# Performance work log

Hardware: AMD Instinct MI355X
Metric: run time of the kernel (lower is better)

The kernel has to match this reference:

```python
import jax, jax.numpy as jnp
import numpy as np

B, T, H = 256, 48, 512   # batch, timesteps, hidden (= size_seq feature dim)
S = H                    # size_seq == hidden feature dim (dim_seq_in = S+1)
K = 4                    # k_wk_ahead


def setup_inputs() -> dict:
    key = jax.random.key(0)
    ks = jax.random.split(key, 20)
    g = lambda k, shp: (jax.random.normal(k, shp, dtype=jnp.float32) * 0.05)
    inp = {
        "hiddens": jax.random.normal(ks[0], (B, T, S), dtype=jnp.float32),
        "allys": jax.random.normal(ks[1], (B, T), dtype=jnp.float32),
        "k_wk_ahead": K,
        # InputAttention params (Linear stored as [in, out])
        "Wh": g(ks[2], (H, S)), "bh": g(ks[3], (S,)),
        "Ws": g(ks[4], (S, S)), "bs": g(ks[5], (S,)),
        "Wo": g(ks[6], (S, 1)), "bo": g(ks[7], (1,)),
        # GRU params (torch layout: [3H, in]/[3H, H], gates ordered r,z,n)
        "W_ih": g(ks[8], (3 * H, S + 1)), "W_hh": g(ks[9], (3 * H, H)),
        "b_ih": g(ks[10], (3 * H,)), "b_hh": g(ks[11], (3 * H,)),
        # out_layer MLP: H->H/2->H/4->H/8->1 with LeakyReLU after each
        "W1": g(ks[12], (H, H // 2)), "b1": g(ks[13], (H // 2,)),
        "W2": g(ks[14], (H // 2, H // 4)), "b2": g(ks[15], (H // 4,)),
        "W3": g(ks[16], (H // 4, H // 8)), "b3": g(ks[17], (H // 8,)),
        "W4": g(ks[18], (H // 8, 1)), "b4": g(ks[19], (1,)),
    }
    return inp


def _gru_step(x, h, W_ih, W_hh, b_ih, b_hh):
    # torch GRU cell: gates ordered (reset, update, new)
    gi = x @ W_ih.T + b_ih          # [B, 3H]
    gh = h @ W_hh.T + b_hh          # [B, 3H]
    ir, iz, inn = jnp.split(gi, 3, axis=-1)
    hr, hz, hn = jnp.split(gh, 3, axis=-1)
    r = jax.nn.sigmoid(ir + hr)
    z = jax.nn.sigmoid(iz + hz)
    n = jnp.tanh(inn + r * hn)
    return (1.0 - z) * n + z * h


def reference(hiddens, allys, k_wk_ahead, Wh, bh, Ws, bs, Wo, bo,
              W_ih, W_hh, b_ih, b_hh, W1, b1, W2, b2, W3, b3, W4, b4):
    Bb, Tt, Ss = hiddens.shape
    # linearSignals(hiddens) is time-step-invariant: precompute once
    ls = hiddens @ Ws + bs                      # [B, T, S]

    def step(d_prev, ally_t):
        lh = d_prev @ Wh + bh                   # [B, S]
        e = jnp.tanh(lh[:, None, :] + ls) @ Wo + bo    # [B, T, 1]
        att = jax.nn.softmax(e, axis=1)[..., 0]        # [B, T]
        c = jnp.einsum('bt,bts->bs', att, hiddens)     # [B, S]
        x = jnp.concatenate([c, ally_t[:, None]], axis=1)   # [B, S+1]
        d = _gru_step(x, d_prev, W_ih, W_hh, b_ih, b_hh)
        return d, c

    d0 = jnp.zeros((Bb, W_hh.shape[1]), dtype=hiddens.dtype)
    d_last, cs = jax.lax.scan(step, d0, jnp.swapaxes(allys, 0, 1))
    c_last = cs[-1]                             # c_vectors[:, -1]

    def mlp(d):
        h = jax.nn.leaky_relu(d @ W1 + b1)
        h = jax.nn.leaky_relu(h @ W2 + b2)
        h = jax.nn.leaky_relu(h @ W3 + b3)
        return jax.nn.leaky_relu(h @ W4 + b4)   # dropout is identity in eval

    outs = []
    last_d = d_last
    for _ in range(k_wk_ahead):
        out = mlp(last_d)                       # [B, 1]
        outs.append(out)
        x = jnp.concatenate([c_last, out], axis=1)
        last_d = _gru_step(x, last_d, W_ih, W_hh, b_ih, b_hh)
    return jnp.stack(outs, axis=1)[..., 0]      # [B, K]
```

## Files before the change

kernel.cpp:

```cpp
#include <hip/hip_runtime.h>
#include <cstdio>

#ifndef __has_builtin
#define __has_builtin(x) 0
#endif

#define NB      256
#define NT      48
#define NS      512
#define KAHEAD  4
#define NTHREADS 1024
#define NBLOCKS  256
#define GSIZE    32
#define RSTRIDE  544
#define XSLOT    512
#define XROWB    1088

#define WS_D     0
#define WS_X     139264
#define WS_LH    278528
#define WS_BAR   409600
#define WS_WA    409856
#define WS_WC    934144
#define WS_WN    1196288
#define WS_WS    1327360
#define WS_WAL   1458432
#define WS_FLOATS 1982720

#define L_XHI    0
#define L_XLO    34816
#define L_LSB    69632
#define L_GH     118784
#define L_GI     125312
#define L_LH     131840
#define L_WO     133888
#define L_E      135936
#define L_ATT    136192
#define L_CP     136448
#define L_H1P    138496
#define L_H1S    142592
#define L_H2P    143616
#define L_H2S    145664
#define L_H3P    146176
#define L_MISC   147200
#define L_PB     147216
#define LDS_BYTES 155408

typedef float    f4v  __attribute__((ext_vector_type(4)));
typedef float    f16v __attribute__((ext_vector_type(16)));
typedef _Float16 h4v  __attribute__((ext_vector_type(4)));
typedef _Float16 h8v  __attribute__((ext_vector_type(8)));

__device__ __forceinline__ f16v MFMA32(h8v a, h8v b, f16v c) {
    return __builtin_amdgcn_mfma_f32_32x32x16_f16(a, b, c, 0, 0, 0);
}
__device__ __forceinline__ f4v MFMA16(h8v a, h8v b, f4v c) {
    return __builtin_amdgcn_mfma_f32_16x16x32_f16(a, b, c, 0, 0, 0);
}

#if __has_builtin(__builtin_bit_cast)
#define F2H_BITS(v) __builtin_bit_cast(h8v, (v))
#define H2F_BITS(v) __builtin_bit_cast(f4v, (v))
#else
__device__ __forceinline__ h8v f2h_bits_(f4v v) { union { f4v f; h8v h; } u; u.f = v; return u.h; }
__device__ __forceinline__ f4v h2f_bits_(h8v v) { union { f4v f; h8v h; } u; u.h = v; return u.f; }
#define F2H_BITS(v) f2h_bits_(v)
#define H2F_BITS(v) h2f_bits_(v)
#endif

__device__ __forceinline__ float frcp_(float x) {
#if __has_builtin(__builtin_amdgcn_rcpf)
    return __builtin_amdgcn_rcpf(x);
#else
    return 1.0f / x;
#endif
}
__device__ __forceinline__ float ftanh_(float x) {
    float e = __expf(2.0f * x);
    return 1.0f - 2.0f * frcp_(e + 1.0f);
}
__device__ __forceinline__ float fsig_(float x) { return frcp_(1.0f + __expf(-x)); }
__device__ __forceinline__ float lrelu_(float x) { return fmaxf(x, 0.01f * x); }
__device__ __forceinline__ void split16_(float v, _Float16& hi, _Float16& lo) {
    _Float16 h = (_Float16)v;
    hi = h;
    lo = (_Float16)(v - (float)h);
}
__device__ __forceinline__ unsigned short f2hbits_(float v) {
    union { _Float16 h; unsigned short u; } c; c.h = (_Float16)v; return c.u;
}
__device__ __forceinline__ float hbits2f_(unsigned short u) {
    union { unsigned short u; _Float16 h; } c; c.u = u; return (float)c.h;
}

__device__ __forceinline__ void cstore1(float* p, float v) {
    asm volatile("global_store_dword %0, %1, off sc0" :: "v"(p), "v"(v) : "memory");
}
__device__ __forceinline__ f4v cload4(const float* p) {
    f4v v;
    asm volatile("global_load_dwordx4 %0, %1, off sc0" : "=v"(v) : "v"(p));
    return v;
}
__device__ __forceinline__ float cload1(const float* p) {
    float v;
    asm volatile("global_load_dword %0, %1, off sc0" : "=v"(v) : "v"(p));
    return v;
}
__device__ __forceinline__ void cwait() {
    asm volatile("s_waitcnt vmcnt(0)" ::: "memory");
    __builtin_amdgcn_sched_barrier(0);
}

__device__ __forceinline__ void gbar(unsigned* bar, unsigned* epoch) {
    asm volatile("s_waitcnt vmcnt(0)" ::: "memory");
    __syncthreads();
    if (threadIdx.x == 0) {
        *epoch += GSIZE;
        __hip_atomic_fetch_add(bar, 1u, __ATOMIC_RELAXED, __HIP_MEMORY_SCOPE_AGENT);
        unsigned target = *epoch;
        int guard = 0;
        while (__hip_atomic_load(bar, __ATOMIC_RELAXED, __HIP_MEMORY_SCOPE_AGENT) < target) {
#if __has_builtin(__builtin_amdgcn_s_sleep)
            __builtin_amdgcn_s_sleep(1);
#endif
            if (++guard > (1 << 17)) break;
        }
    }
    __syncthreads();
}

__device__ __forceinline__ void cvtStore_(char* hiB, char* loB, int idx, f4v v) {
    unsigned row = (unsigned)idx / 544u;
    unsigned col = (unsigned)idx - row * 544u;
    h4v h, l;
    #pragma unroll
    for (int i = 0; i < 4; ++i) { _Float16 hh, ll; split16_(v[i], hh, ll); h[i] = hh; l[i] = ll; }
    *(h4v*)(hiB + row * XROWB + col * 2) = h;
    *(h4v*)(loB + row * XROWB + col * 2) = l;
}
__device__ __forceinline__ void stagePanel(const float* __restrict__ gsrc,
                                           char* __restrict__ hiB,
                                           char* __restrict__ loB, int tid) {
    f4v v0 = cload4(gsrc + tid * 4);
    f4v v1 = cload4(gsrc + 4096 + tid * 4);
    f4v v2 = cload4(gsrc + 8192 + tid * 4);
    f4v v3 = cload4(gsrc + 12288 + tid * 4);
    f4v v4 = {0.f, 0.f, 0.f, 0.f};
    if (tid < 256) v4 = cload4(gsrc + 16384 + tid * 4);
    cwait();
    cvtStore_(hiB, loB, tid * 4, v0);
    cvtStore_(hiB, loB, 4096 + tid * 4, v1);
    cvtStore_(hiB, loB, 8192 + tid * 4, v2);
    cvtStore_(hiB, loB, 12288 + tid * 4, v3);
    if (tid < 256) cvtStore_(hiB, loB, 16384 + tid * 4, v4);
}

#define DO_GEMMA(doLH) do {                                                          \
    f16v acc_ = (f16v){0,0,0,0,0,0,0,0,0,0,0,0,0,0,0,0};                             \
    if (w < 4) {                                                                     \
        const int kc_ = w >> 1;                                                      \
        const int aoff_ = (l & 31) * XROWB + ((l >> 5) << 4);                        \
        _Pragma("unroll")                                                            \
        for (int kt = 0; kt < 16; ++kt) {                                            \
            h8v ah = *(const h8v*)(smem + L_XHI + aoff_ + (kc_ * 16 + kt) * 32);     \
            h8v al = *(const h8v*)(smem + L_XLO + aoff_ + (kc_ * 16 + kt) * 32);     \
            acc_ = MFMA32(ah, wreg[kt], acc_);                                       \
            acc_ = MFMA32(al, wreg[kt], acc_);                                       \
        }                                                                            \
        const _Float16* blp_ = walF +                                                \
            ((long)((cix * 2 + (w & 1)) * 32 + kc_ * 16)) * 512 + (l << 3);          \
        _Pragma("unroll 4")                                                          \
        for (int kt = 0; kt < 16; ++kt) {                                            \
            h8v ah = *(const h8v*)(smem + L_XHI + aoff_ + (kc_ * 16 + kt) * 32);     \
            h8v bl8 = *(const h8v*)(blp_ + kt * 512);                                \
            acc_ = MFMA32(ah, bl8, acc_);                                            \
        }                                                                            \
        if (kc_ == 1) {                                                              \
            _Pragma("unroll")                                                        \
            for (int r = 0; r < 16; ++r) pbuf[(w & 1) * 1024 + r * 64 + l] = acc_[r];\
        }                                                                            \
    }                                                                                \
    __syncthreads();                                                                 \
    if (w < 2) {                                                                     \
        _Pragma("unroll")                                                            \
        for (int r = 0; r < 16; ++r) acc_[r] += pbuf[w * 1024 + r * 64 + l];         \
        const int c_ = w * 32 + (l & 31);                                            \
        const int rb_ = (l >> 5) << 2;                                               \
        if (c_ < 16) {                                                               \
            if (doLH) {                                                              \
                const int j_ = cix * 16 + c_;                                        \
                const float bb_ = bh[j_];                                            \
                _Pragma("unroll")                                                    \
                for (int r = 0; r < 16; ++r) {                                       \
                    int row_ = (r & 3) + ((r >> 2) << 3) + rb_;                      \
                    cstore1(lhw + (long)(g * 32 + row_) * NS + j_, acc_[r] + bb_);   \
                }                                                                    \
            }                                                                        \
        } else {                                                                     \
            const int gate_ = (c_ - 16) >> 4, jj_ = (c_ - 16) & 15;                  \
            const float bb_ = b_hh[gate_ * 512 + cix * 16 + jj_];                    \
            _Pragma("unroll")                                                        \
            for (int r = 0; r < 16; ++r) {                                           \
                int row_ = (r & 3) + ((r >> 2) << 3) + rb_;                          \
                ghs[gate_ * 544 + row_ * 17 + jj_] = acc_[r] + bb_;                  \
            }                                                                        \
        }                                                                            \
    }                                                                                \
} while (0)

#define DO_GEMMC() do {                                                              \
    f16v acc_ = (f16v){0,0,0,0,0,0,0,0,0,0,0,0,0,0,0,0};                             \
    f4v an0_ = {0.f,0.f,0.f,0.f}, an1_ = {0.f,0.f,0.f,0.f};                          \
    if (w == 4 || w == 5) {                                                          \
        const int kc_ = w - 4;                                                       \
        const int aoff_ = (l & 31) * XROWB + ((l >> 5) << 4);                        \
        _Pragma("unroll")                                                            \
        for (int kt = 0; kt < 16; ++kt) {                                            \
            h8v ah = *(const h8v*)(smem + L_XHI + aoff_ + (kc_ * 16 + kt) * 32);     \
            h8v al = *(const h8v*)(smem + L_XLO + aoff_ + (kc_ * 16 + kt) * 32);     \
            acc_ = MFMA32(ah, wreg[kt], acc_);                                       \
            acc_ = MFMA32(al, wreg[kt], acc_);                                       \
        }                                                                            \
        if (kc_ == 1) {                                                              \
            _Pragma("unroll")                                                        \
            for (int r = 0; r < 16; ++r) pbuf[r * 64 + l] = acc_[r];                 \
        }                                                                            \
    } else if (w == 6 || w == 7) {                                                   \
        const int kc_ = w - 6;                                                       \
        const int a0_ = (l & 15) * XROWB + ((l >> 4) << 4);                          \
        const int a1_ = a0_ + 16 * XROWB;                                            \
        _Pragma("unroll")                                                            \
        for (int kt = 0; kt < 8; ++kt) {                                             \
            const int kb_ = (kc_ * 8 + kt) * 64;                                     \
            h8v ah0 = *(const h8v*)(smem + L_XHI + a0_ + kb_);                       \
            h8v al0 = *(const h8v*)(smem + L_XLO + a0_ + kb_);                       \
            h8v ah1 = *(const h8v*)(smem + L_XHI + a1_ + kb_);                       \
            h8v al1 = *(const h8v*)(smem + L_XLO + a1_ + kb_);                       \
            an0_ = MFMA16(ah0, wreg[kt], an0_); an0_ = MFMA16(al0, wreg[kt], an0_);  \
            an1_ = MFMA16(ah1, wreg[kt], an1_); an1_ = MFMA16(al1, wreg[kt], an1_);  \
        }                                                                            \
        if (kc_ == 1) {                                                              \
            _Pragma("unroll")                                                        \
            for (int r = 0; r < 4; ++r) {                                            \
                pbuf[1024 + r * 64 + l] = an0_[r];                                   \
                pbuf[1280 + r * 64 + l] = an1_[r];                                   \
            }                                                                        \
        }                                                                            \
    }                                                                                \
    __syncthreads();                                                                 \
    if (w == 4) {                                                                    \
        _Pragma("unroll")                                                            \
        for (int r = 0; r < 16; ++r) acc_[r] += pbuf[r * 64 + l];                    \
        const int c_ = l & 31, gate_ = c_ >> 4, jj_ = c_ & 15;                       \
        const int rb_ = (l >> 5) << 2;                                               \
        const float bb_ = b_ih[gate_ * 512 + cix * 16 + jj_];                        \
        _Pragma("unroll")                                                            \
        for (int r = 0; r < 16; ++r) {                                               \
            int row_ = (r & 3) + ((r >> 2) << 3) + rb_;                              \
            gis[gate_ * 544 + row_ * 17 + jj_] = acc_[r] + bb_;                      \
        }                                                                            \
    } else if (w == 6) {                                                             \
        const int jj_ = l & 15;                                                      \
        const float bb_ = b_ih[1024 + cix * 16 + jj_];                               \
        _Pragma("unroll")                                                            \
        for (int r = 0; r < 4; ++r) {                                                \
            int row_ = ((l >> 4) << 2) + r;                                          \
            gis[1088 + row_ * 17 + jj_] = an0_[r] + pbuf[1024 + r * 64 + l] + bb_;   \
            gis[1088 + (16 + row_) * 17 + jj_] = an1_[r] + pbuf[1280 + r * 64 + l] + bb_; \
        }                                                                            \
    }                                                                                \
} while (0)

__device__ __forceinline__ void lsGemm(const char* smem, const _Float16* WS_,
        int tid, int ch, unsigned short* lsb, const float* bs) {
    const int w = tid >> 6, l = tid & 63;
    const int mt = w & 1, ng = w >> 1;
    const int aoff = (mt * 16 + (l & 15)) * XROWB + ((l >> 4) << 4);
    f4v acc[4] = {{0,0,0,0},{0,0,0,0},{0,0,0,0},{0,0,0,0}};
    for (int kt = 0; kt < 16; ++kt) {
        h8v ah = *(const h8v*)(smem + L_XHI + aoff + kt * 64);
        h8v al = *(const h8v*)(smem + L_XLO + aoff + kt * 64);
        #pragma unroll
        for (int i = 0; i < 4; ++i) {
            const _Float16* bp = WS_ + ((long)((ng * 4 + i) * 16 + kt)) * 512 + (l << 3);
            h8v bb = *(const h8v*)bp;
            acc[i] = MFMA16(ah, bb, acc[i]);
            acc[i] = MFMA16(al, bb, acc[i]);
        }
    }
    #pragma unroll
    for (int i = 0; i < 4; ++i) {
        const int n = (ng * 4 + i) * 16 + (l & 15);
        const float bsv = bs[n];
        #pragma unroll
        for (int r = 0; r < 4; ++r) {
            int row = mt * 16 + ((l >> 4) << 2) + r;
            if (row < 24)
                lsb[(ch * 24 + row) * NS + n] = f2hbits_(acc[i][r] + bsv);
        }
    }
}

__global__ void prep_kernel(const float* __restrict__ Whh,
                            const float* __restrict__ Wih,
                            const float* __restrict__ Wh,
                            const float* __restrict__ Ws,
                            float* __restrict__ ws) {
    long i = (long)blockIdx.x * blockDim.x + threadIdx.x;
    long stride = (long)gridDim.x * blockDim.x;
    _Float16* wa  = (_Float16*)(ws + WS_WA);
    _Float16* wal = (_Float16*)(ws + WS_WAL);
    _Float16* wc  = (_Float16*)(ws + WS_WC);
    _Float16* wn  = (_Float16*)(ws + WS_WN);
    _Float16* wsls = (_Float16*)(ws + WS_WS);

    for (long p = i; p < 131072; p += stride) {
        int l = (int)(p & 63);
        long t = p >> 6;
        int kt = (int)(t & 31);
        int u = (int)(t >> 5);
        int nt = u & 1, cix = u >> 1;
        int c = nt * 32 + (l & 31);
        #pragma unroll
        for (int e = 0; e < 8; ++e) {
            int k = kt * 16 + ((l >> 5) << 3) + e;
            float wv;
            if (c < 16) wv = Wh[(long)k * 512 + cix * 16 + c];
            else {
                int gate = (c - 16) >> 4, j = cix * 16 + ((c - 16) & 15);
                wv = Whh[((long)(gate * 512 + j)) * 512 + k];
            }
            _Float16 hv = (_Float16)wv;
            wa[p * 8 + e]  = hv;
            wal[p * 8 + e] = (_Float16)(wv - (float)hv);
        }
    }
    for (long p = i; p < 65536; p += stride) {
        int l = (int)(p & 63);
        long t = p >> 6;
        int kt = (int)(t & 31), cix = (int)(t >> 5);
        int c = l & 31, gate = c >> 4, j = cix * 16 + (c & 15);
        #pragma unroll
        for (int e = 0; e < 8; ++e) {
            int k = kt * 16 + ((l >> 5) << 3) + e;
            wc[p * 8 + e] = (_Float16)Wih[((long)(gate * 512 + j)) * 513 + k];
        }
    }
    for (long p = i; p < 32768; p += stride) {
        int l = (int)(p & 63);
        long t = p >> 6;
        int kt = (int)(t & 15), cix = (int)(t >> 4);
        int j = cix * 16 + (l & 15);
        #pragma unroll
        for (int e = 0; e < 8; ++e) {
            int k = kt * 32 + ((l >> 4) << 3) + e;
            wn[p * 8 + e] = (_Float16)Wih[((long)(1024 + j)) * 513 + k];
        }
    }
    for (long p = i; p < 32768; p += stride) {
        int l = (int)(p & 63);
        long t = p >> 6;
        int kt = (int)(t & 15), nt = (int)(t >> 4);
        int n = nt * 16 + (l & 15);
        #pragma unroll
        for (int e = 0; e < 8; ++e) {
            int k = kt * 32 + ((l >> 4) << 3) + e;
            wsls[p * 8 + e] = (_Float16)Ws[(long)k * 512 + n];
        }
    }
    for (long p = i; p < 278528; p += stride) ws[WS_D + p] = 0.0f;
    if (i < 256) ((unsigned*)(ws + WS_BAR))[i] = 0u;
}

__global__ void __launch_bounds__(NTHREADS, 4) fused_kernel(
        const float* __restrict__ hiddens, const float* __restrict__ allys,
        const float* __restrict__ bs,
        const float* __restrict__ Wo, const float* __restrict__ bo,
        const float* __restrict__ bh,
        const float* __restrict__ b_ih, const float* __restrict__ b_hh,
        const float* __restrict__ Wih,
        const float* __restrict__ W1, const float* __restrict__ b1,
        const float* __restrict__ W2, const float* __restrict__ b2,
        const float* __restrict__ W3, const float* __restrict__ b3,
        const float* __restrict__ W4, const float* __restrict__ b4,
        float* __restrict__ ws, float* __restrict__ out) {
    const int tid = threadIdx.x;

    float* dw  = ws + WS_D;
    float* xw  = ws + WS_X;
    float* lhw = ws + WS_LH;
    const _Float16* waF  = (const _Float16*)(ws + WS_WA);
    const _Float16* walF = (const _Float16*)(ws + WS_WAL);
    const _Float16* wcF  = (const _Float16*)(ws + WS_WC);
    const _Float16* wnF  = (const _Float16*)(ws + WS_WN);
    const _Float16* wsF  = (const _Float16*)(ws + WS_WS);
    unsigned* barbase = (unsigned*)(ws + WS_BAR);

    extern __shared__ char smem[];
    char*           xhi   = smem + L_XHI;
    char*           xlo   = smem + L_XLO;
    unsigned short* lsb   = (unsigned short*)(smem + L_LSB);
    float*          ghs   = (float*)(smem + L_GH);
    float*          gis   = (float*)(smem + L_GI);
    float*          lh_s  = (float*)(smem + L_LH);
    float*          wo_s  = (float*)(smem + L_WO);
    float*          e_s   = (float*)(smem + L_E);
    float*          att_s = (float*)(smem + L_ATT);
    float*          h1p   = (float*)(smem + L_H1P);
    float*          h1s   = (float*)(smem + L_H1S);
    float*          h2p   = (float*)(smem + L_H2P);
    float*          h2s   = (float*)(smem + L_H2S);
    float*          h3p   = (float*)(smem + L_H3P);
    int*            misc  = (int*)(smem + L_MISC);
    float*          pbuf  = (float*)(smem + L_PB);

    if (tid == 0) {
        unsigned xcc;
        asm volatile("s_getreg_b32 %0, hwreg(HW_REG_XCC_ID)" : "=s"(xcc));
        int gx = (int)(xcc & 7u);
        unsigned rk = __hip_atomic_fetch_add(barbase + gx * 32 + 1, 1u,
                                             __ATOMIC_RELAXED, __HIP_MEMORY_SCOPE_AGENT);
        misc[0] = gx;
        misc[1] = (int)(rk & 31u);
    }
    __syncthreads();
    const int g = misc[0], cix = misc[1];
    const int myb = g * 32 + cix;
    unsigned* bar = barbase + (g << 5);
    unsigned epoch = 0;

    const int w = tid >> 6, l = tid & 63;
    const int sS = tid & 511;
    const int rowE = tid >> 4, jE = tid & 15;
    const int jgE = cix * 16 + jE;
    const float* gPanelD = dw + (long)g * GSIZE * RSTRIDE;
    const float* gPanelX = xw + (long)g * GSIZE * RSTRIDE;

    float w512r = 0.f, w512z = 0.f, w512n = 0.f;
    if (tid < 512) {
        w512r = Wih[(long)jgE * 513 + 512];
        w512z = Wih[(long)(512 + jgE) * 513 + 512];
        w512n = Wih[(long)(1024 + jgE) * 513 + 512];
    }

    if (tid < NS) wo_s[tid] = Wo[tid];

    for (int i = tid; i < 4352; i += NTHREADS) *(f4v*)(smem + i * 16) = (f4v){0,0,0,0};
    for (int ch = 0; ch < 2; ++ch) {
        __syncthreads();
        {
            const float* src = hiddens + ((long)myb * NT + ch * 24) * NS;
            const int i0 = tid * 12;
            #pragma unroll
            for (int j3 = 0; j3 < 3; ++j3) {
                int idx = i0 + j3 * 4;
                f4v v = *(const f4v*)(src + idx);
                int row = idx >> 9, col = idx & 511;
                h4v h, lo;
                #pragma unroll
                for (int e = 0; e < 4; ++e) { _Float16 hh, ll; split16_(v[e], hh, ll); h[e] = hh; lo[e] = ll; }
                *(h4v*)(xhi + row * XROWB + col * 2) = h;
                *(h4v*)(xlo + row * XROWB + col * 2) = lo;
            }
        }
        __syncthreads();
        lsGemm(smem, wsF, tid, ch, lsb, bs);
    }
    __syncthreads();

    h8v wreg[16];
    if (w < 4) {
        const _Float16* p = waF + ((long)((cix * 2 + (w & 1)) * 32 + (w >> 1) * 16)) * 512 + (l << 3);
        #pragma unroll
        for (int kt = 0; kt < 16; ++kt) wreg[kt] = *(const h8v*)(p + kt * 512);
    } else if (w < 6) {
        const _Float16* p = wcF + ((long)(cix * 32 + (w - 4) * 16)) * 512 + (l << 3);
        #pragma unroll
        for (int kt = 0; kt < 16; ++kt) wreg[kt] = *(const h8v*)(p + kt * 512);
    } else if (w < 8) {
        const _Float16* p = wnF + ((long)(cix * 16 + (w - 6) * 8)) * 512 + (l << 3);
        #pragma unroll
        for (int kt = 0; kt < 8; ++kt) wreg[kt] = *(const h8v*)(p + kt * 512);
    } else {
        const float* hb = hiddens + (long)myb * NT * NS + sS;
        #pragma unroll
        for (int q = 0; q < 12; ++q) {
            f4v v = { hb[(q * 4 + 0) * 512], hb[(q * 4 + 1) * 512],
                      hb[(q * 4 + 2) * 512], hb[(q * 4 + 3) * 512] };
            wreg[q] = F2H_BITS(v);
        }
    }

    const float bo0 = bo[0];

    for (int t = 0; t < NT; ++t) {
        stagePanel(gPanelD, xhi, xlo, tid);
        __syncthreads();
        DO_GEMMA(true);
        gbar(bar, &epoch);

        if (tid < 128) {
            f4v v = cload4(lhw + (long)myb * NS + tid * 4);
            cwait();
            *(f4v*)(lh_s + tid * 4) = v;
        }
        if (tid == 0) cstore1(xw + (long)myb * RSTRIDE + XSLOT, allys[myb * NT + t]);
        __syncthreads();
        {
            const int wv = tid >> 6, ln = tid & 63;
            for (int q = 0; q < 3; ++q) {
                const int tt = wv * 3 + q;
                float p = 0.f;
                #pragma unroll
                for (int i2 = 0; i2 < 8; ++i2) {
                    int s = ln + (i2 << 6);
                    p = fmaf(wo_s[s], ftanh_(lh_s[s] + hbits2f_(lsb[tt * NS + s])), p);
                }
                #pragma unroll
                for (int off = 32; off >= 1; off >>= 1) p += __shfl_xor(p, off, 64);
                if (ln == 0) e_s[tt] = p + bo0;
            }
        }
        __syncthreads();
        if (tid < 64) {
            float v = (tid < NT) ? e_s[tid] : -1e30f;
            float m = v;
            #pragma unroll
            for (int off = 32; off >= 1; off >>= 1) m = fmaxf(m, __shfl_xor(m, off, 64));
            float ex = (tid < NT) ? __expf(v - m) : 0.0f;
            float ssum = ex;
            #pragma unroll
            for (int off = 32; off >= 1; off >>= 1) ssum += __shfl_xor(ssum, off, 64);
            if (tid < NT) att_s[tid] = ex * frcp_(ssum);
        }
        __syncthreads();
        if (tid >= 512) {
            float c = 0.f;
            #pragma unroll
            for (int q = 0; q < 12; ++q) {
                f4v hv = H2F_BITS(wreg[q]);
                c = fmaf(att_s[q * 4 + 0], hv.x, c);
                c = fmaf(att_s[q * 4 + 1], hv.y, c);
                c = fmaf(att_s[q * 4 + 2], hv.z, c);
                c = fmaf(att_s[q * 4 + 3], hv.w, c);
            }
            cstore1(xw + (long)myb * RSTRIDE + sS, c);
        }
        gbar(bar, &epoch);

        float hp = 0.f;
        if (tid < 512) hp = cload1(dw + (long)(g * 32 + rowE) * RSTRIDE + jgE);
        stagePanel(gPanelX, xhi, xlo, tid);
        __syncthreads();
        DO_GEMMC();
        __syncthreads();
        if (tid < 512) {
            float x512f = (float)*(const _Float16*)(xhi + rowE * XROWB + 1024)
                        + (float)*(const _Float16*)(xlo + rowE * XROWB + 1024);
            float gr  = fmaf(x512f, w512r, gis[rowE * 17 + jE]        + ghs[rowE * 17 + jE]);
            float gz  = fmaf(x512f, w512z, gis[544 + rowE * 17 + jE]  + ghs[544 + rowE * 17 + jE]);
            float gni = fmaf(x512f, w512n, gis[1088 + rowE * 17 + jE]);
            float gnh = ghs[1088 + rowE * 17 + jE];
            float rg = fsig_(gr);
            float zg = fsig_(gz);
            float ng = ftanh_(fmaf(rg, gnh, gni));
            cstore1(dw + (long)(g * 32 + rowE) * RSTRIDE + jgE, (1.f - zg) * ng + zg * hp);
        }
        gbar(bar, &epoch);
    }

    for (int kk = 0; kk < KAHEAD; ++kk) {
        {
            float v = 0.f;
            if (tid < NS) v = cload1(dw + (long)myb * RSTRIDE + tid);
            cwait();
            if (tid < NS) lh_s[tid] = v;
        }
        __syncthreads();
        {
            int n = tid & 255, q4 = tid >> 8;
            const float* av = lh_s + q4 * 128;
            const float* wp = W1 + (long)(q4 * 128) * 256 + n;
            float acc = 0.f;
            #pragma unroll 4
            for (int k2 = 0; k2 < 128; ++k2) { acc = fmaf(av[k2], wp[0], acc); wp += 256; }
            h1p[n * 4 + q4] = acc;
        }
        __syncthreads();
        if (tid < 256) {
            float v = h1p[tid * 4] + h1p[tid * 4 + 1] + h1p[tid * 4 + 2] + h1p[tid * 4 + 3];
            h1s[tid] = lrelu_(v + b1[tid]);
        }
        __syncthreads();
        if (tid < 512) {
            int n = tid & 127, q4 = tid >> 7;
            const float* av = h1s + q4 * 64;
            const float* wp = W2 + (long)(q4 * 64) * 128 + n;
            float acc = 0.f;
            #pragma unroll 4
            for (int k2 = 0; k2 < 64; ++k2) { acc = fmaf(av[k2], wp[0], acc); wp += 128; }
            h2p[n * 4 + q4] = acc;
        }
        __syncthreads();
        if (tid < 128) {
            float v = h2p[tid * 4] + h2p[tid * 4 + 1] + h2p[tid * 4 + 2] + h2p[tid * 4 + 3];
            h2s[tid] = lrelu_(v + b2[tid]);
        }
        __syncthreads();
        if (tid < 256) {
            int n = tid & 63, q4 = tid >> 6;
            const float* av = h2s + q4 * 32;
            const float* wp = W3 + (long)(q4 * 32) * 64 + n;
            float acc = 0.f;
            #pragma unroll 4
            for (int k2 = 0; k2 < 32; ++k2) { acc = fmaf(av[k2], wp[0], acc); wp += 64; }
            h3p[n * 4 + q4] = acc;
        }
        __syncthreads();
        if (tid < 64) {
            float v = h3p[tid * 4] + h3p[tid * 4 + 1] + h3p[tid * 4 + 2] + h3p[tid * 4 + 3];
            float h3v = lrelu_(v + b3[tid]);
            float p = h3v * W4[tid];
            #pragma unroll
            for (int off = 32; off >= 1; off >>= 1) p += __shfl_xor(p, off, 64);
            if (tid == 0) {
                float o = lrelu_(p + b4[0]);
                out[myb * KAHEAD + kk] = o;
                cstore1(xw + (long)myb * RSTRIDE + XSLOT, o);
            }
        }
        if (kk < KAHEAD - 1) {
            gbar(bar, &epoch);
            float hp = 0.f;
            if (tid < 512) hp = cload1(dw + (long)(g * 32 + rowE) * RSTRIDE + jgE);
            stagePanel(gPanelD, xhi, xlo, tid);
            __syncthreads();
            DO_GEMMA(false);
            __syncthreads();
            stagePanel(gPanelX, xhi, xlo, tid);
            __syncthreads();
            DO_GEMMC();
            __syncthreads();
            if (tid < 512) {
                float x512f = (float)*(const _Float16*)(xhi + rowE * XROWB + 1024)
                            + (float)*(const _Float16*)(xlo + rowE * XROWB + 1024);
                float gr  = fmaf(x512f, w512r, gis[rowE * 17 + jE]        + ghs[rowE * 17 + jE]);
                float gz  = fmaf(x512f, w512z, gis[544 + rowE * 17 + jE]  + ghs[544 + rowE * 17 + jE]);
                float gni = fmaf(x512f, w512n, gis[1088 + rowE * 17 + jE]);
                float gnh = ghs[1088 + rowE * 17 + jE];
                float rg = fsig_(gr);
                float zg = fsig_(gz);
                float ng = ftanh_(fmaf(rg, gnh, gni));
                cstore1(dw + (long)(g * 32 + rowE) * RSTRIDE + jgE, (1.f - zg) * ng + zg * hp);
            }
            gbar(bar, &epoch);
        }
    }
}

extern "C" void kernel_launch(void* const* d_in, const int* in_sizes, int n_in,
                              void* d_out, int out_size, void* d_ws, size_t ws_size,
                              hipStream_t stream) {
    const float* hiddens = (const float*)d_in[0];
    const float* allys   = (const float*)d_in[1];
    const float* Wh   = (const float*)d_in[3];
    const float* bh   = (const float*)d_in[4];
    const float* Ws   = (const float*)d_in[5];
    const float* bs   = (const float*)d_in[6];
    const float* Wo   = (const float*)d_in[7];
    const float* bo   = (const float*)d_in[8];
    const float* W_ih = (const float*)d_in[9];
    const float* W_hh = (const float*)d_in[10];
    const float* b_ih = (const float*)d_in[11];
    const float* b_hh = (const float*)d_in[12];
    const float* W1 = (const float*)d_in[13];
    const float* b1 = (const float*)d_in[14];
    const float* W2 = (const float*)d_in[15];
    const float* b2 = (const float*)d_in[16];
    const float* W3 = (const float*)d_in[17];
    const float* b3 = (const float*)d_in[18];
    const float* W4 = (const float*)d_in[19];
    const float* b4 = (const float*)d_in[20];
    float* wsf = (float*)d_ws;
    float* outf = (float*)d_out;

    if (ws_size < (size_t)WS_FLOATS * sizeof(float)) {
        fprintf(stderr, "kernel_launch: workspace too small (%zu < %zu)\n",
                ws_size, (size_t)WS_FLOATS * sizeof(float));
        return;
    }

    prep_kernel<<<dim3(2048), dim3(256), 0, stream>>>(W_hh, W_ih, Wh, Ws, wsf);

    (void)hipFuncSetAttribute((const void*)fused_kernel,
                              hipFuncAttributeMaxDynamicSharedMemorySize, LDS_BYTES);

    void* args[] = { &hiddens, &allys, &bs, &Wo, &bo, &bh,
                     &b_ih, &b_hh, &W_ih, &W1, &b1, &W2, &b2, &W3, &b3, &W4, &b4,
                     &wsf, &outf };
    hipError_t e = hipLaunchCooperativeKernel((void*)fused_kernel,
                                              dim3(NBLOCKS), dim3(NTHREADS),
                                              args, LDS_BYTES, stream);
    if (e != hipSuccess) {
        fprintf(stderr, "coop launch failed (%d); plain fallback\n", (int)e);
        (void)hipGetLastError();
        fused_kernel<<<dim3(NBLOCKS), dim3(NTHREADS), LDS_BYTES, stream>>>(
            hiddens, allys, bs, Wo, bo, bh, b_ih, b_hh, W_ih,
            W1, b1, W2, b2, W3, b3, W4, b4, wsf, outf);
    }
}
```

Before: 1.980 ms.

## Compute attention projection locally per block, removing grid barrier and lh exchange

Each block now computes its own batch row's d_prev @ Wh with packed fp16 dot2 instructions over a new pair-packed Wh layout, on waves that were idle during the GRU hidden GEMM. This removes the global store of lh, one grid-wide barrier per timestep and the reload of lh from global memory. The low-half correction term for W_hh is dropped, so the hidden GEMM now uses single fp16 weights, trading some precision for fewer MFMAs. The LDS row stride is padded, which should reduce bank conflicts on the row reads of the new loop.

New measurement: 3.615 ms. 1.83x slower.

```diff
diff --git a/kernel.cpp b/kernel.cpp
--- a/kernel.cpp
+++ b/kernel.cpp
@@ -14,7 +14,7 @@
 #define GSIZE    32
 #define RSTRIDE  544
 #define XSLOT    512
-#define XROWB    1088
+#define XROWB    1104
 
 #define WS_D     0
 #define WS_X     139264
@@ -24,30 +24,31 @@
 #define WS_WC    934144
 #define WS_WN    1196288
 #define WS_WS    1327360
-#define WS_WAL   1458432
-#define WS_FLOATS 1982720
+#define WS_WHF   1458432
+#define WS_FLOATS 1589504
 
 #define L_XHI    0
-#define L_XLO    34816
-#define L_LSB    69632
-#define L_GH     118784
-#define L_GI     125312
-#define L_LH     131840
-#define L_WO     133888
-#define L_E      135936
-#define L_ATT    136192
-#define L_CP     136448
-#define L_H1P    138496
-#define L_H1S    142592
-#define L_H2P    143616
-#define L_H2S    145664
-#define L_H3P    146176
-#define L_MISC   147200
-#define L_PB     147216
-#define LDS_BYTES 155408
+#define L_XLO    35328
+#define L_LSB    70656
+#define L_GH     119808
+#define L_GI     126336
+#define L_LH     132864
+#define L_WO     134912
+#define L_E      136960
+#define L_ATT    137216
+#define L_CP     137472
+#define L_H1P    139520
+#define L_H1S    143616
+#define L_H2P    144640
+#define L_H2S    146688
+#define L_H3P    147200
+#define L_MISC   148224
+#define L_PB     148240
+#define LDS_BYTES 156432
 
 typedef float    f4v  __attribute__((ext_vector_type(4)));
 typedef float    f16v __attribute__((ext_vector_type(16)));
+typedef _Float16 h2v  __attribute__((ext_vector_type(2)));
 typedef _Float16 h4v  __attribute__((ext_vector_type(4)));
 typedef _Float16 h8v  __attribute__((ext_vector_type(8)));
 
@@ -67,6 +68,15 @@
 #define F2H_BITS(v) f2h_bits_(v)
 #define H2F_BITS(v) h2f_bits_(v)
 #endif
+
+__device__ __forceinline__ h2v u2h2_(unsigned u) { union { unsigned u; h2v h; } c; c.u = u; return c.h; }
+__device__ __forceinline__ float fdot2_(h2v a, h2v b, float c) {
+#if __has_builtin(__builtin_amdgcn_fdot2)
+    return __builtin_amdgcn_fdot2(a, b, c, false);
+#else
+    return fmaf((float)a[0], (float)b[0], fmaf((float)a[1], (float)b[1], c));
+#endif
+}
 
 __device__ __forceinline__ float frcp_(float x) {
 #if __has_builtin(__builtin_amdgcn_rcpf)
@@ -155,7 +165,7 @@
     if (tid < 256) cvtStore_(hiB, loB, 16384 + tid * 4, v4);
 }
 
-#define DO_GEMMA(doLH) do {                                                          \
+#define DO_GEMMA() do {                                                              \
     f16v acc_ = (f16v){0,0,0,0,0,0,0,0,0,0,0,0,0,0,0,0};                             \
     if (w < 4) {                                                                     \
         const int kc_ = w >> 1;                                                      \
@@ -167,18 +177,21 @@
             acc_ = MFMA32(ah, wreg[kt], acc_);                                       \
             acc_ = MFMA32(al, wreg[kt], acc_);                                       \
         }                                                                            \
-        const _Float16* blp_ = walF +                                                \
-            ((long)((cix * 2 + (w & 1)) * 32 + kc_ * 16)) * 512 + (l << 3);          \
-        _Pragma("unroll 4")                                                          \
-        for (int kt = 0; kt < 16; ++kt) {                                            \
-            h8v ah = *(const h8v*)(smem + L_XHI + aoff_ + (kc_ * 16 + kt) * 32);     \
-            h8v bl8 = *(const h8v*)(blp_ + kt * 512);                                \
-            acc_ = MFMA32(ah, bl8, acc_);                                            \
-        }                                                                            \
         if (kc_ == 1) {                                                              \
             _Pragma("unroll")                                                        \
             for (int r = 0; r < 16; ++r) pbuf[(w & 1) * 1024 + r * 64 + l] = acc_[r];\
         }                                                                            \
+    } else if (w < 12) {                                                             \
+        const int j_ = tid - 256;                                                    \
+        const unsigned* dru_ = (const unsigned*)(smem + L_XHI + cix * XROWB);        \
+        const unsigned* wp_ = whf2 + j_;                                             \
+        float accl_ = bh[j_];                                                        \
+        _Pragma("unroll 8")                                                          \
+        for (int k2 = 0; k2 < 256; ++k2) {                                           \
+            accl_ = fdot2_(u2h2_(dru_[k2]), u2h2_(wp_[0]), accl_);                   \
+            wp_ += 512;                                                              \
+        }                                                                            \
+        lh_s[j_] = accl_;                                                            \
     }                                                                                \
     __syncthreads();                                                                 \
     if (w < 2) {                                                                     \
@@ -186,17 +199,42 @@
         for (int r = 0; r < 16; ++r) acc_[r] += pbuf[w * 1024 + r * 64 + l];         \
         const int c_ = w * 32 + (l & 31);                                            \
         const int rb_ = (l >> 5) << 2;                                               \
-        if (c_ < 16) {                                                               \
-            if (doLH) {                                                              \
-                const int j_ = cix * 16 + c_;                                        \
-                const float bb_ = bh[j_];                                            \
-                _Pragma("unroll")                                                    \
-                for (int r = 0; r < 16; ++r) {                                       \
-                    int row_ = (r & 3) + ((r >> 2) << 3) + rb_;                      \
-                    cstore1(lhw + (long)(g * 32 + row_) * NS + j_, acc_[r] + bb_);   \
-                }                                                                    \
+        if (c_ >= 16) {                                                              \
+            const int gate_ = (c_ - 16) >> 4, jj_ = (c_ - 16) & 15;                  \
+            const float bb_ = b_hh[gate_ * 512 + cix * 16 + jj_];                    \
+            _Pragma("unroll")                                                        \
+            for (int r = 0; r < 16; ++r) {                                           \
+                int row_ = (r & 3) + ((r >> 2) << 3) + rb_;                          \
+                ghs[gate_ * 544 + row_ * 17 + jj_] = acc_[r] + bb_;                  \
             }                                                                        \
-        } else {                                                                     \
+        }                                                                            \
+    }                                                                                \
+} while (0)
+
+#define DO_GEMMA_NOLH() do {                                                         \
+    f16v acc_ = (f16v){0,0,0,0,0,0,0,0,0,0,0,0,0,0,0,0};                             \
+    if (w < 4) {                                                                     \
+        const int kc_ = w >> 1;                                                      \
+        const int aoff_ = (l & 31) * XROWB + ((l >> 5) << 4);                        \
+        _Pragma("unroll")                                                            \
+        for (int kt = 0; kt < 16; ++kt) {                                            \
+            h8v ah = *(const h8v*)(smem + L_XHI + aoff_ + (kc_ * 16 + kt) * 32);     \
+            h8v al = *(const h8v*)(smem + L_XLO + aoff_ + (kc_ * 16 + kt) * 32);     \
+            acc_ = MFMA32(ah, wreg[kt], acc_);                                       \
+            acc_ = MFMA32(al, wreg[kt], acc_);                                       \
+        }                                                                            \
+        if (kc_ == 1) {                                                              \
+            _Pragma("unroll")                                                        \
+            for (int r = 0; r < 16; ++r) pbuf[(w & 1) * 1024 + r * 64 + l] = acc_[r];\
+        }                                                                            \
+    }                                                                                \
+    __syncthreads();                                                                 \
+    if (w < 2) {                                                                     \
+        _Pragma("unroll")                                                            \
+        for (int r = 0; r < 16; ++r) acc_[r] += pbuf[w * 1024 + r * 64 + l];         \
+        const int c_ = w * 32 + (l & 31);                                            \
+        const int rb_ = (l >> 5) << 2;                                               \
+        if (c_ >= 16) {                                                              \
             const int gate_ = (c_ - 16) >> 4, jj_ = (c_ - 16) & 15;                  \
             const float bb_ = b_hh[gate_ * 512 + cix * 16 + jj_];                    \
             _Pragma("unroll")                                                        \
@@ -309,10 +347,10 @@
     long i = (long)blockIdx.x * blockDim.x + threadIdx.x;
     long stride = (long)gridDim.x * blockDim.x;
     _Float16* wa  = (_Float16*)(ws + WS_WA);
-    _Float16* wal = (_Float16*)(ws + WS_WAL);
     _Float16* wc  = (_Float16*)(ws + WS_WC);
     _Float16* wn  = (_Float16*)(ws + WS_WN);
     _Float16* wsls = (_Float16*)(ws + WS_WS);
+    unsigned* whf2 = (unsigned*)(ws + WS_WHF);
 
     for (long p = i; p < 131072; p += stride) {
         int l = (int)(p & 63);
@@ -330,9 +368,7 @@
                 int gate = (c - 16) >> 4, j = cix * 16 + ((c - 16) & 15);
                 wv = Whh[((long)(gate * 512 + j)) * 512 + k];
             }
-            _Float16 hv = (_Float16)wv;
-            wa[p * 8 + e]  = hv;
-            wal[p * 8 + e] = (_Float16)(wv - (float)hv);
+            wa[p * 8 + e] = (_Float16)wv;
         }
     }
     for (long p = i; p < 65536; p += stride) {
@@ -367,6 +403,13 @@
             int k = kt * 32 + ((l >> 4) << 3) + e;
             wsls[p * 8 + e] = (_Float16)Ws[(long)k * 512 + n];
         }
+    }
+    for (long p = i; p < 131072; p += stride) {
+        int j = (int)(p & 511), k2 = (int)(p >> 9);
+        union { _Float16 h[2]; unsigned u; } c;
+        c.h[0] = (_Float16)Wh[(long)(2 * k2) * 512 + j];
+        c.h[1] = (_Float16)Wh[(long)(2 * k2 + 1) * 512 + j];
+        whf2[p] = c.u;
     }
     for (long p = i; p < 278528; p += stride) ws[WS_D + p] = 0.0f;
     if (i < 256) ((unsigned*)(ws + WS_BAR))[i] = 0u;
@@ -388,12 +431,11 @@
 
     float* dw  = ws + WS_D;
     float* xw  = ws + WS_X;
-    float* lhw = ws + WS_LH;
     const _Float16* waF  = (const _Float16*)(ws + WS_WA);
-    const _Float16* walF = (const _Float16*)(ws + WS_WAL);
     const _Float16* wcF  = (const _Float16*)(ws + WS_WC);
     const _Float16* wnF  = (const _Float16*)(ws + WS_WN);
     const _Float16* wsF  = (const _Float16*)(ws + WS_WS);
+    const unsigned* whf2 = (const unsigned*)(ws + WS_WHF);
     unsigned* barbase = (unsigned*)(ws + WS_BAR);
 
     extern __shared__ char smem[];
@@ -430,7 +472,7 @@
     unsigned epoch = 0;
 
     const int w = tid >> 6, l = tid & 63;
-    const int sS = tid & 511;
+    const int sS = tid & 511, th = tid >> 9;
     const int rowE = tid >> 4, jE = tid & 15;
     const int jgE = cix * 16 + jE;
     const float* gPanelD = dw + (long)g * GSIZE * RSTRIDE;
@@ -445,7 +487,7 @@
 
     if (tid < NS) wo_s[tid] = Wo[tid];
 
-    for (int i = tid; i < 4352; i += NTHREADS) *(f4v*)(smem + i * 16) = (f4v){0,0,0,0};
+    for (int i = tid; i < 4416; i += NTHREADS) *(f4v*)(smem + i * 16) = (f4v){0,0,0,0};
     for (int ch = 0; ch < 2; ++ch) {
         __syncthreads();
         {
@@ -496,16 +538,8 @@
     for (int t = 0; t < NT; ++t) {
         stagePanel(gPanelD, xhi, xlo, tid);
         __syncthreads();
-        DO_GEMMA(true);
-        gbar(bar, &epoch);
-
-        if (tid < 128) {
-            f4v v = cload4(lhw + (long)myb * NS + tid * 4);
-            cwait();
-            *(f4v*)(lh_s + tid * 4) = v;
-        }
+        DO_GEMMA();
         if (tid == 0) cstore1(xw + (long)myb * RSTRIDE + XSLOT, allys[myb * NT + t]);
-        __syncthreads();
         {
             const int wv = tid >> 6, ln = tid & 63;
             for (int q = 0; q < 3; ++q) {
@@ -635,7 +669,7 @@
             if (tid < 512) hp = cload1(dw + (long)(g * 32 + rowE) * RSTRIDE + jgE);
             stagePanel(gPanelD, xhi, xlo, tid);
             __syncthreads();
-            DO_GEMMA(false);
+            DO_GEMMA_NOLH();
             __syncthreads();
             stagePanel(gPanelX, xhi, xlo, tid);
             __syncthreads();
```
